# Optimization experiments

Measured on AMD Instinct MI355X. Metric: run time of the kernel, lower is better.

## Reference

```python
import jax, jax.numpy as jnp
import numpy as np

V, TB, L, H, D, HD, FF = 50257, 1024, 6, 12, 768, 64, 4 * 768
B, T = 2, 1024
EOS = 50256


def _layernorm(x, g, b, eps=1e-5):
    mu = x.mean(-1, keepdims=True)
    var = ((x - mu) ** 2).mean(-1, keepdims=True)
    return (x - mu) * jax.lax.rsqrt(var + eps) * g + b


def setup_inputs() -> dict:
    key = jax.random.key(0)
    ks = jax.random.split(key, 10)
    resid_std = 0.02 * (2 * L) ** (-0.5)

    def n(k, shape, std=0.02):
        return (std * jax.random.normal(k, shape)).astype(jnp.float32)

    return {
        "idx": jax.random.randint(ks[0], (B, T), 0, V, dtype=jnp.int32),
        "targets": jax.random.randint(ks[1], (B, T), 0, V, dtype=jnp.int32),
        "token_emb": n(ks[2], (V, D)),           # tied with head
        "pos_emb": n(ks[3], (1, TB, D)),
        "ln1_g": jnp.ones((L, D), jnp.float32),
        "ln1_b": jnp.zeros((L, D), jnp.float32),
        "ln2_g": jnp.ones((L, D), jnp.float32),
        "ln2_b": jnp.zeros((L, D), jnp.float32),
        "W_qkv": n(ks[4], (L, D, 3 * D)),
        "b_qkv": jnp.zeros((L, 3 * D), jnp.float32),
        "W_proj": n(ks[5], (L, D, D), resid_std),
        "b_proj": jnp.zeros((L, D), jnp.float32),
        "W_fc1": n(ks[6], (L, D, FF)),
        "b_fc1": jnp.zeros((L, FF), jnp.float32),
        "W_fc2": n(ks[7], (L, FF, D), resid_std),
        "b_fc2": jnp.zeros((L, D), jnp.float32),
        "lnf_g": jnp.ones((D,), jnp.float32),
        "lnf_b": jnp.zeros((D,), jnp.float32),
    }


def reference(idx, targets, token_emb, pos_emb, ln1_g, ln1_b, ln2_g, ln2_b,
              W_qkv, b_qkv, W_proj, b_proj, W_fc1, b_fc1, W_fc2, b_fc2,
              lnf_g, lnf_b):
    Bc, Tc = idx.shape
    x = token_emb[idx] + pos_emb[:, :Tc, :]  # [B,T,D]; dropout=0 -> identity

    # document-boundary causal mask: same_doc & causal
    is_eos = (idx == EOS).astype(jnp.int32)
    doc_id = jnp.cumsum(is_eos, axis=1) - is_eos          # [B,T]
    same_doc = doc_id[:, :, None] == doc_id[:, None, :]   # [B,T,T]
    causal = jnp.tril(jnp.ones((Tc, Tc), dtype=bool))
    mask = same_doc & causal                               # [B,T,T]
    scale = 1.0 / float(np.sqrt(HD))

    def block(x, p):
        g1, b1, Wq, bq, Wp, bp, g2, b2, Wf1, bf1, Wf2, bf2 = p
        h = _layernorm(x, g1, b1)
        qkv = (h @ Wq + bq).reshape(Bc, Tc, 3, H, HD)
        q = qkv[:, :, 0].transpose(0, 2, 1, 3)  # [B,H,T,hd]
        k = qkv[:, :, 1].transpose(0, 2, 1, 3)
        v = qkv[:, :, 2].transpose(0, 2, 1, 3)
        att = jnp.einsum('bhqd,bhkd->bhqk', q, k) * scale
        att = jnp.where(mask[:, None, :, :], att, -jnp.inf)
        att = jax.nn.softmax(att, axis=-1)
        y = jnp.einsum('bhqk,bhkd->bhqd', att, v)
        y = y.transpose(0, 2, 1, 3).reshape(Bc, Tc, D)
        x = x + (y @ Wp + bp)
        h2 = _layernorm(x, g2, b2)
        x = x + (jax.nn.gelu(h2 @ Wf1 + bf1, approximate=False) @ Wf2 + bf2)
        return x, None

    x, _ = jax.lax.scan(block, x, (ln1_g, ln1_b, W_qkv, b_qkv, W_proj, b_proj,
                                   ln2_g, ln2_b, W_fc1, b_fc1, W_fc2, b_fc2))
    x = _layernorm(x, lnf_g, lnf_b)
    logits = x @ token_emb.T  # tied head, no bias
    logp = jax.nn.log_softmax(logits, axis=-1)
    tgt = targets.astype(jnp.int32)[..., None]
    loss = -jnp.take_along_axis(logp, tgt, axis=-1).mean()
    return logits, loss
```

## Files before the change

### kernel.cpp

```cpp
#include <hip/hip_runtime.h>
#include <hip/hip_bf16.h>
#include <math.h>

#define V_ 50257
#define L_ 6
#define H_ 12
#define D_ 768
#define HD_ 64
#define FF_ 3072
#define B_ 2
#define T_ 1024
#define NTOK (B_*T_)
#define EOS_ 50256
#define QBLK 64
#define KVB 64
#define NS2 393
#define QS3 (3*D_)

typedef __attribute__((ext_vector_type(8))) short s16x8;
typedef __attribute__((ext_vector_type(4))) short s16x4;
typedef __attribute__((ext_vector_type(4))) float f32x4;

__device__ __forceinline__ short f2bf(float f) {
  __hip_bfloat16 h = __float2bfloat16(f);
  return *reinterpret_cast<short*>(&h);
}

__device__ __forceinline__ void gl_lds16(const void* g, void* l) {
  __builtin_amdgcn_global_load_lds(
      (const __attribute__((address_space(1))) unsigned int*)g,
      (__attribute__((address_space(3))) unsigned int*)l, 16, 0, 0);
}

__global__ void k_embed(const int* __restrict__ idx, const float* __restrict__ tok,
                        const float* __restrict__ pos, float* __restrict__ x) {
  int gid = blockIdx.x * blockDim.x + threadIdx.x;
  const int total = NTOK * D_;
  if (gid >= total) return;
  int row = gid / D_;
  int d = gid - row * D_;
  int t = row & (T_ - 1);
  x[gid] = tok[(size_t)idx[row] * D_ + d] + pos[t * D_ + d];
}

__global__ void k_docid(const int* __restrict__ idx, int* __restrict__ doc) {
  int b = threadIdx.x;
  if (b >= B_) return;
  int c = 0;
  for (int t = 0; t < T_; ++t) {
    int e = (idx[b*T_ + t] == EOS_) ? 1 : 0;
    doc[b*T_ + t] = c;
    c += e;
  }
}

__global__ void k_cast_tok(const float* __restrict__ in,
                           __hip_bfloat16* __restrict__ out, long n8) {
  long i = (long)blockIdx.x*blockDim.x + threadIdx.x;
  long stride = (long)gridDim.x*blockDim.x;
  for (; i < n8; i += stride) {
    const float4* src = (const float4*)(in + i*8);
    float4 v0 = src[0], v1 = src[1];
    s16x8 s;
    s[0]=f2bf(v0.x); s[1]=f2bf(v0.y); s[2]=f2bf(v0.z); s[3]=f2bf(v0.w);
    s[4]=f2bf(v1.x); s[5]=f2bf(v1.y); s[6]=f2bf(v1.z); s[7]=f2bf(v1.w);
    *(s16x8*)((short*)out + i*8) = s;
  }
}

__global__ __launch_bounds__(256) void k_ln(
    const float* __restrict__ x, const float* __restrict__ g,
    const float* __restrict__ b, __hip_bfloat16* __restrict__ out) {
  int row = blockIdx.x * 4 + (threadIdx.x >> 6);
  int lane = threadIdx.x & 63;
  const float* xr = x + (size_t)row * D_;
  float4 v[3];
  float s = 0.f;
  #pragma unroll
  for (int i = 0; i < 3; ++i) {
    v[i] = *(const float4*)(xr + lane*4 + i*256);
    s += v[i].x + v[i].y + v[i].z + v[i].w;
  }
  #pragma unroll
  for (int o = 1; o < 64; o <<= 1) s += __shfl_xor(s, o);
  float mu = s * (1.f/D_);
  float var = 0.f;
  #pragma unroll
  for (int i = 0; i < 3; ++i) {
    float a0=v[i].x-mu, a1=v[i].y-mu, a2=v[i].z-mu, a3=v[i].w-mu;
    var += a0*a0 + a1*a1 + a2*a2 + a3*a3;
  }
  #pragma unroll
  for (int o = 1; o < 64; o <<= 1) var += __shfl_xor(var, o);
  float inv = rsqrtf(var * (1.f/D_) + 1e-5f);
  #pragma unroll
  for (int i = 0; i < 3; ++i) {
    int d = lane*4 + i*256;
    float4 gg = *(const float4*)(g + d);
    float4 bb = *(const float4*)(b + d);
    s16x4 o4;
    o4[0] = f2bf((v[i].x-mu)*inv*gg.x + bb.x);
    o4[1] = f2bf((v[i].y-mu)*inv*gg.y + bb.y);
    o4[2] = f2bf((v[i].z-mu)*inv*gg.z + bb.z);
    o4[3] = f2bf((v[i].w-mu)*inv*gg.w + bb.w);
    *(s16x4*)((short*)out + (size_t)row*D_ + d) = o4;
  }
}

__global__ void k_wt(const float* __restrict__ in, __hip_bfloat16* __restrict__ out,
                     int K, int N) {
  __shared__ float tile[32][33];
  int l = blockIdx.z;
  const float* src = in + (size_t)l*K*N;
  __hip_bfloat16* dst = out + (size_t)l*N*K;
  int n0 = blockIdx.x*32, k0 = blockIdx.y*32;
  int tx = threadIdx.x, ty = threadIdx.y;
  #pragma unroll
  for (int i = 0; i < 4; ++i)
    tile[ty + i*8][tx] = src[(size_t)(k0 + ty + i*8)*N + n0 + tx];
  __syncthreads();
  #pragma unroll
  for (int i = 0; i < 4; ++i)
    dst[(size_t)(n0 + ty + i*8)*K + k0 + tx] = __float2bfloat16(tile[tx][ty + i*8]);
}

__global__ __launch_bounds__(256) void k_mfma_nt(
    const __hip_bfloat16* __restrict__ A,
    const __hip_bfloat16* __restrict__ Bh,
    const float* __restrict__ Bf,
    const float* __restrict__ bias,
    const float* resid,
    float* outf, __hip_bfloat16* outh,
    int M, int N, int K, int gelu)
{
  __shared__ __align__(16) short lds_a[2*128*64];
  __shared__ __align__(16) short lds_b[2*64*64];
  const int t = threadIdx.x;
  const int m0 = blockIdx.y * 128;
  const int n0 = blockIdx.x * 64;
  const int lane = t & 63;
  const int wid = t >> 6;
  const int wm = (wid >> 1) * 64;
  const int wn = (wid & 1) * 32;
  const int lrow = lane & 15;
  const int lkb = (lane >> 4) * 16;
  const int wbase = (t & 192) * 16;

  int offA[4][2], offB[2][2];
  #pragma unroll
  for (int f = 0; f < 4; ++f)
    #pragma unroll
    for (int ks = 0; ks < 2; ++ks) {
      int row = wm + f*16 + lrow;
      offA[f][ks] = (row*128 + ks*64 + lkb) ^ ((row & 7) << 4);
    }
  #pragma unroll
  for (int f = 0; f < 2; ++f)
    #pragma unroll
    for (int ks = 0; ks < 2; ++ks) {
      int row = wn + f*16 + lrow;
      offB[f][ks] = (row*128 + ks*64 + lkb) ^ ((row & 7) << 4);
    }

  const char* srcA[4];
  #pragma unroll
  for (int p = 0; p < 4; ++p) {
    int c = p*256 + t;
    int row = c >> 3;
    int colb = (c & 7) << 4;
    srcA[p] = (const char*)A + (size_t)(m0+row)*K*2 + (colb ^ ((row & 7) << 4));
  }
  const char* srcB[2];
  #pragma unroll
  for (int p = 0; p < 2; ++p) {
    int c = p*256 + t;
    int row = c >> 3;
    int colb = (c & 7) << 4;
    srcB[p] = Bh ? ((const char*)Bh + (size_t)(n0+row)*K*2 + (colb ^ ((row & 7) << 4)))
                 : nullptr;
  }

  auto stageA = [&](int boff, int k0) {
    #pragma unroll
    for (int p = 0; p < 4; ++p)
      gl_lds16(srcA[p] + k0*2, (char*)lds_a + boff + p*4096 + wbase);
  };
  auto stageB = [&](int boff, int k0) {
    if (Bh) {
      #pragma unroll
      for (int p = 0; p < 2; ++p)
        gl_lds16(srcB[p] + k0*2, (char*)lds_b + boff + p*4096 + wbase);
    } else {
      #pragma unroll
      for (int p = 0; p < 2; ++p) {
        int c = p*256 + t;
        int row = c >> 3;
        int colb = (c & 7) << 4;
        int gn = n0 + row;
        s16x8 s = {0,0,0,0,0,0,0,0};
        if (gn < N) {
          const char* src = (const char*)Bf + ((size_t)gn*K + k0)*4 + colb*2;
          float4 v0 = *(const float4*)src;
          float4 v1 = *(const float4*)(src + 16);
          s[0]=f2bf(v0.x); s[1]=f2bf(v0.y); s[2]=f2bf(v0.z); s[3]=f2bf(v0.w);
          s[4]=f2bf(v1.x); s[5]=f2bf(v1.y); s[6]=f2bf(v1.z); s[7]=f2bf(v1.w);
        }
        int dst = (row*128 + colb) ^ ((row & 7) << 4);
        *(s16x8*)((char*)lds_b + boff + dst) = s;
      }
    }
  };

  f32x4 acc[4][2];
  #pragma unroll
  for (int i = 0; i < 4; ++i)
    #pragma unroll
    for (int j = 0; j < 2; ++j)
      acc[i][j] = (f32x4){0.f, 0.f, 0.f, 0.f};

  const int nk = K >> 6;
  stageA(0, 0);       stageB(0, 0);
  stageA(1<<14, 64);  stageB(1<<13, 64);
  const bool piped = (Bh != nullptr);
  for (int kt = 0; kt < nk; ++kt) {
    if (piped && kt + 1 < nk) asm volatile("s_waitcnt vmcnt(6)" ::: "memory");
    else                      asm volatile("s_waitcnt vmcnt(0) lgkmcnt(0)" ::: "memory");
    __builtin_amdgcn_s_barrier();
    const int ba = (kt & 1) << 14;
    const int bb = (kt & 1) << 13;
    #pragma unroll
    for (int ks = 0; ks < 2; ++ks) {
      s16x8 af[4], bfr[2];
      #pragma unroll
      for (int f = 0; f < 4; ++f)
        af[f] = *(const s16x8*)((const char*)lds_a + ba + offA[f][ks]);
      #pragma unroll
      for (int f = 0; f < 2; ++f)
        bfr[f] = *(const s16x8*)((const char*)lds_b + bb + offB[f][ks]);
      #pragma unroll
      for (int fm = 0; fm < 4; ++fm)
        #pragma unroll
        for (int fn = 0; fn < 2; ++fn)
          acc[fm][fn] = __builtin_amdgcn_mfma_f32_16x16x32_bf16(
              af[fm], bfr[fn], acc[fm][fn], 0, 0, 0);
    }
    __builtin_amdgcn_s_barrier();
    if (kt + 2 < nk) { stageA(ba, (kt+2)*64); stageB(bb, (kt+2)*64); }
  }
  const int crow = (lane >> 4) * 4;
  #pragma unroll
  for (int fm = 0; fm < 4; ++fm) {
    #pragma unroll
    for (int fn = 0; fn < 2; ++fn) {
      int col = n0 + wn + fn*16 + lrow;
      if (col >= N) continue;
      #pragma unroll
      for (int r = 0; r < 4; ++r) {
        int row = m0 + wm + fm*16 + crow + r;
        float v = acc[fm][fn][r];
        if (bias) v += bias[col];
        if (gelu) v = 0.5f * v * (1.f + erff(v * 0.70710678118654752f));
        if (resid) v += resid[(size_t)row*N + col];
        if (outf) outf[(size_t)row*N + col] = v;
        else      outh[(size_t)row*N + col] = __float2bfloat16(v);
      }
    }
  }
}

__global__ __launch_bounds__(256) void k_mfma_nt64(
    const __hip_bfloat16* __restrict__ A,
    const __hip_bfloat16* __restrict__ Bh,
    const float* __restrict__ bias,
    const float* resid,
    float* outf,
    int M, int N, int K)
{
  __shared__ __align__(16) short lds_a[2][64*64];
  __shared__ __align__(16) short lds_b[2][64*64];
  const int t = threadIdx.x;
  const int m0 = blockIdx.y * 64;
  const int n0 = blockIdx.x * 64;
  const int lane = t & 63;
  const int wid = t >> 6;
  const int wm = (wid >> 1) * 32;
  const int wn = (wid & 1) * 32;
  const int lrow = lane & 15;
  const int lkb = (lane >> 4) * 16;
  const int wbase = (t & 192) * 16;

  auto stage = [&](int buf, int k0) {
    #pragma unroll
    for (int p = 0; p < 2; ++p) {
      int c = p*256 + t;
      int row = c >> 3;
      int colb = (c & 7) << 4;
      const char* srcA = (const char*)A + ((size_t)(m0+row)*K + k0)*2 + (colb ^ ((row & 7) << 4));
      gl_lds16(srcA, (char*)lds_a[buf] + p*4096 + wbase);
    }
    #pragma unroll
    for (int p = 0; p < 2; ++p) {
      int c = p*256 + t;
      int row = c >> 3;
      int colb = (c & 7) << 4;
      const char* srcB = (const char*)Bh + ((size_t)(n0+row)*K + k0)*2 + (colb ^ ((row & 7) << 4));
      gl_lds16(srcB, (char*)lds_b[buf] + p*4096 + wbase);
    }
  };

  f32x4 acc[2][2];
  #pragma unroll
  for (int i = 0; i < 2; ++i)
    #pragma unroll
    for (int j = 0; j < 2; ++j)
      acc[i][j] = (f32x4){0.f, 0.f, 0.f, 0.f};

  const int nk = K >> 6;
  stage(0, 0);
  stage(1, 64);
  for (int kt = 0; kt < nk; ++kt) {
    if (kt + 1 < nk) asm volatile("s_waitcnt vmcnt(4)" ::: "memory");
    else             asm volatile("s_waitcnt vmcnt(0)" ::: "memory");
    __builtin_amdgcn_s_barrier();
    const int cur = kt & 1;
    #pragma unroll
    for (int ks = 0; ks < 2; ++ks) {
      s16x8 af[2], bfr[2];
      #pragma unroll
      for (int f = 0; f < 2; ++f) {
        int row = wm + f*16 + lrow;
        int off = (row*128 + ks*64 + lkb) ^ ((row & 7) << 4);
        af[f] = *(const s16x8*)((const char*)lds_a[cur] + off);
      }
      #pragma unroll
      for (int f = 0; f < 2; ++f) {
        int row = wn + f*16 + lrow;
        int off = (row*128 + ks*64 + lkb) ^ ((row & 7) << 4);
        bfr[f] = *(const s16x8*)((const char*)lds_b[cur] + off);
      }
      #pragma unroll
      for (int fm = 0; fm < 2; ++fm)
        #pragma unroll
        for (int fn = 0; fn < 2; ++fn)
          acc[fm][fn] = __builtin_amdgcn_mfma_f32_16x16x32_bf16(
              af[fm], bfr[fn], acc[fm][fn], 0, 0, 0);
    }
    __builtin_amdgcn_s_barrier();
    if (kt + 2 < nk) stage(cur, (kt+2)*64);
  }
  const int crow = (lane >> 4) * 4;
  #pragma unroll
  for (int fm = 0; fm < 2; ++fm) {
    #pragma unroll
    for (int fn = 0; fn < 2; ++fn) {
      int col = n0 + wn + fn*16 + lrow;
      #pragma unroll
      for (int r = 0; r < 4; ++r) {
        int row = m0 + wm + fm*16 + crow + r;
        float v = acc[fm][fn][r] + bias[col];
        if (resid) v += resid[(size_t)row*N + col];
        outf[(size_t)row*N + col] = v;
      }
    }
  }
}

__global__ __launch_bounds__(512) void k_logits(
    const __hip_bfloat16* __restrict__ A,
    const __hip_bfloat16* __restrict__ Bh,
    const float* __restrict__ Bf,
    float* __restrict__ C,
    float2* __restrict__ part)
{
  __shared__ __align__(16) short lds_a[2*128*64];
  __shared__ __align__(16) short lds_b[2*128*64];
  const int t = threadIdx.x;
  const int bid = blockIdx.x;
  const int lid = (bid & 7) * (NS2*16/8) + (bid >> 3);
  const int m0 = (lid & 15) * 128;
  const int nt = lid >> 4;
  const int n0 = nt * 128;
  const int lane = t & 63;
  const int wid = t >> 6;
  const int wm = (wid >> 2) * 64;
  const int wn = (wid & 3) * 32;
  const int lrow = lane & 15;
  const int lkb = (lane >> 4) * 16;
  const int wbase = (t & 448) * 16;

  int offA[4][2], offB[2][2];
  #pragma unroll
  for (int f = 0; f < 4; ++f)
    #pragma unroll
    for (int ks = 0; ks < 2; ++ks) {
      int row = wm + f*16 + lrow;
      offA[f][ks] = (row*128 + ks*64 + lkb) ^ ((row & 7) << 4);
    }
  #pragma unroll
  for (int f = 0; f < 2; ++f)
    #pragma unroll
    for (int ks = 0; ks < 2; ++ks) {
      int row = wn + f*16 + lrow;
      offB[f][ks] = (row*128 + ks*64 + lkb) ^ ((row & 7) << 4);
    }

  const char* srcA[2];
  const char* srcB[2];
  #pragma unroll
  for (int p = 0; p < 2; ++p) {
    int c = p*512 + t;
    int row = c >> 3;
    int colb = (c & 7) << 4;
    srcA[p] = (const char*)A + (size_t)(m0+row)*768*2 + (colb ^ ((row & 7) << 4));
    srcB[p] = Bh ? ((const char*)Bh + (size_t)(n0+row)*768*2 + (colb ^ ((row & 7) << 4)))
                 : nullptr;
  }

  auto stageA = [&](int boff, int k0) {
    #pragma unroll
    for (int p = 0; p < 2; ++p)
      gl_lds16(srcA[p] + k0*2, (char*)lds_a + boff + p*8192 + wbase);
  };
  auto stageB = [&](int boff, int k0) {
    if (Bh) {
      #pragma unroll
      for (int p = 0; p < 2; ++p)
        gl_lds16(srcB[p] + k0*2, (char*)lds_b + boff + p*8192 + wbase);
    } else {
      #pragma unroll
      for (int p = 0; p < 2; ++p) {
        int c = p*512 + t;
        int row = c >> 3;
        int colb = (c & 7) << 4;
        int gn = n0 + row;
        s16x8 s = {0,0,0,0,0,0,0,0};
        if (gn < V_) {
          const char* src = (const char*)Bf + ((size_t)gn*768 + k0)*4 + colb*2;
          float4 v0 = *(const float4*)src;
          float4 v1 = *(const float4*)(src + 16);
          s[0]=f2bf(v0.x); s[1]=f2bf(v0.y); s[2]=f2bf(v0.z); s[3]=f2bf(v0.w);
          s[4]=f2bf(v1.x); s[5]=f2bf(v1.y); s[6]=f2bf(v1.z); s[7]=f2bf(v1.w);
        }
        int dst = (row*128 + colb) ^ ((row & 7) << 4);
        *(s16x8*)((char*)lds_b + boff + dst) = s;
      }
    }
  };

  f32x4 acc[4][2];
  #pragma unroll
  for (int i = 0; i < 4; ++i)
    #pragma unroll
    for (int j = 0; j < 2; ++j)
      acc[i][j] = (f32x4){0.f, 0.f, 0.f, 0.f};

  stageA(0, 0);       stageB(0, 0);
  stageA(1<<14, 64);  stageB(1<<14, 64);
  const bool piped = (Bh != nullptr);
  for (int kt = 0; kt < 12; ++kt) {
    if (piped && kt + 1 < 12) asm volatile("s_waitcnt vmcnt(4)" ::: "memory");
    else                      asm volatile("s_waitcnt vmcnt(0) lgkmcnt(0)" ::: "memory");
    __builtin_amdgcn_s_barrier();
    const int boff = (kt & 1) << 14;
    #pragma unroll
    for (int ks = 0; ks < 2; ++ks) {
      s16x8 af[4], bfr[2];
      #pragma unroll
      for (int f = 0; f < 4; ++f)
        af[f] = *(const s16x8*)((const char*)lds_a + boff + offA[f][ks]);
      #pragma unroll
      for (int f = 0; f < 2; ++f)
        bfr[f] = *(const s16x8*)((const char*)lds_b + boff + offB[f][ks]);
      #pragma unroll
      for (int fm = 0; fm < 4; ++fm)
        #pragma unroll
        for (int fn = 0; fn < 2; ++fn)
          acc[fm][fn] = __builtin_amdgcn_mfma_f32_16x16x32_bf16(
              af[fm], bfr[fn], acc[fm][fn], 0, 0, 0);
    }
    __builtin_amdgcn_s_barrier();
    if (kt + 2 < 12) { stageA(boff, (kt+2)*64); stageB(boff, (kt+2)*64); }
  }
  const int crow = (lane >> 4) * 4;
  bool valid[2];
  #pragma unroll
  for (int fn = 0; fn < 2; ++fn) valid[fn] = (n0 + wn + fn*16 + lrow) < V_;
  float2* red = (float2*)lds_a;
  #pragma unroll
  for (int fm = 0; fm < 4; ++fm) {
    #pragma unroll
    for (int r = 0; r < 4; ++r) {
      int rit = wm + fm*16 + crow + r;
      int row = m0 + rit;
      float m = -1e30f;
      #pragma unroll
      for (int fn = 0; fn < 2; ++fn) {
        if (valid[fn]) {
          float v = acc[fm][fn][r];
          C[(size_t)row*V_ + n0 + wn + fn*16 + lrow] = v;
          m = fmaxf(m, v);
        }
      }
      #pragma unroll
      for (int o = 1; o < 16; o <<= 1) m = fmaxf(m, __shfl_xor(m, o));
      float s = 0.f;
      #pragma unroll
      for (int fn = 0; fn < 2; ++fn)
        if (valid[fn]) s += __expf(acc[fm][fn][r] - m);
      #pragma unroll
      for (int o = 1; o < 16; o <<= 1) s += __shfl_xor(s, o);
      if (lrow == 0) red[rit*4 + (wid & 3)] = make_float2(m, s);
    }
  }
  __syncthreads();
  if (t < 128) {
    float M = -1e30f, S = 0.f;
    #pragma unroll
    for (int wc = 0; wc < 4; ++wc) {
      float2 p = red[t*4 + wc];
      float mn = fmaxf(M, p.x);
      S = S*__expf(M - mn) + p.y*__expf(p.x - mn);
      M = mn;
    }
    part[(size_t)(m0 + t)*NS2 + nt] = make_float2(M, S);
  }
}

__global__ void k_rowloss2(const float2* __restrict__ part,
                           const float* __restrict__ logits,
                           const int* __restrict__ tgt, float* __restrict__ rl) {
  int row = blockIdx.x;
  int lane = threadIdx.x;
  float M = -1e30f, S = 0.f;
  for (int i = lane; i < NS2; i += 64) {
    float2 p = part[(size_t)row*NS2 + i];
    float mn = fmaxf(M, p.x);
    S = S*__expf(M - mn) + p.y*__expf(p.x - mn);
    M = mn;
  }
  #pragma unroll
  for (int o = 1; o < 64; o <<= 1) {
    float Mo = __shfl_xor(M, o);
    float So = __shfl_xor(S, o);
    float mn = fmaxf(M, Mo);
    S = S*__expf(M - mn) + So*__expf(Mo - mn);
    M = mn;
  }
  if (lane == 0)
    rl[row] = (logf(S) + M) - logits[(size_t)row*V_ + tgt[row]];
}

__global__ __launch_bounds__(256) void k_fattn(
    const __hip_bfloat16* __restrict__ qkv, const int* __restrict__ doc,
    __hip_bfloat16* __restrict__ y)
{
  __shared__ __align__(16) short q_lds[QBLK*64];
  __shared__ __align__(16) short k_lds[2][KVB*64];
  __shared__ __align__(16) short vt_lds[2][64*KVB];
  __shared__ __align__(16) short p_lds[4][16*64];
  __shared__ int doc_lds[T_];
  const int t = threadIdx.x;
  const int lane = t & 63;
  const int w = t >> 6;
  const int q0 = (gridDim.x - 1 - blockIdx.x) * QBLK;
  const int h = blockIdx.y, b = blockIdx.z;
  const int lrow = lane & 15;
  const int lgrp = lane >> 4;
  const int crow = lgrp * 4;
  const int wbase = (t & 192) * 16;
  const short* qp = (const short*)qkv;

  auto stageK = [&](int kv0, int buf) {
    #pragma unroll
    for (int p = 0; p < 2; ++p) {
      int c = p*256 + t;
      int row = c >> 3;
      int colb = (c & 7) << 4;
      const char* src = (const char*)(qp + ((size_t)(b*T_ + kv0 + row))*QS3 + D_ + h*HD_)
                        + (colb ^ ((row & 7) << 4));
      gl_lds16(src, (char*)k_lds[buf] + p*4096 + wbase);
    }
  };

  #pragma unroll
  for (int p = 0; p < 2; ++p) {
    int c = p*256 + t;
    int row = c >> 3;
    int colb = (c & 7) << 4;
    const char* src = (const char*)(qp + ((size_t)(b*T_ + q0 + row))*QS3 + h*HD_)
                      + (colb ^ ((row & 7) << 4));
    gl_lds16(src, (char*)q_lds + p*4096 + wbase);
  }
  #pragma unroll
  for (int i = 0; i < 4; ++i) doc_lds[t + i*256] = doc[b*T_ + t + i*256];
  stageK(0, 0);
  s16x8 vc0, vc1;
  {
    int c0 = t, c1 = 256 + t;
    vc0 = *(const s16x8*)(qp + ((size_t)(b*T_ + (c0>>3)))*QS3 + 2*D_ + h*HD_ + (c0&7)*8);
    vc1 = *(const s16x8*)(qp + ((size_t)(b*T_ + (c1>>3)))*QS3 + 2*D_ + h*HD_ + (c1&7)*8);
  }
  __syncthreads();

  int docq[4];
  #pragma unroll
  for (int r = 0; r < 4; ++r)
    docq[r] = doc_lds[q0 + w*16 + crow + r];

  float m_r[4], l_r[4];
  #pragma unroll
  for (int r = 0; r < 4; ++r) { m_r[r] = -1e30f; l_r[r] = 0.f; }
  f32x4 o[4];
  #pragma unroll
  for (int fd = 0; fd < 4; ++fd) o[fd] = (f32x4){0.f,0.f,0.f,0.f};

  const int ntiles = q0/KVB + 1;
  for (int kt = 0; kt < ntiles; ++kt) {
    const int kv0 = kt * KVB;
    const int cur = kt & 1;
    const bool hn = (kt + 1 < ntiles);
    s16x8 vn0, vn1;
    if (hn) {
      stageK(kv0 + KVB, cur ^ 1);
      int c0 = t, c1 = 256 + t;
      vn0 = *(const s16x8*)(qp + ((size_t)(b*T_ + kv0 + KVB + (c0>>3)))*QS3 + 2*D_ + h*HD_ + (c0&7)*8);
      vn1 = *(const s16x8*)(qp + ((size_t)(b*T_ + kv0 + KVB + (c1>>3)))*QS3 + 2*D_ + h*HD_ + (c1&7)*8);
    }
    {
      int c0 = t, kvr0 = c0 >> 3, d00 = (c0 & 7)*8;
      #pragma unroll
      for (int j = 0; j < 8; ++j) {
        int d = d00 + j;
        int off = (d*128 + kvr0*2) ^ ((d & 7) << 4);
        *(short*)((char*)vt_lds[cur] + off) = vc0[j];
      }
      int c1 = 256 + t, kvr1 = c1 >> 3, d01 = (c1 & 7)*8;
      #pragma unroll
      for (int j = 0; j < 8; ++j) {
        int d = d01 + j;
        int off = (d*128 + kvr1*2) ^ ((d & 7) << 4);
        *(short*)((char*)vt_lds[cur] + off) = vc1[j];
      }
    }
    if (hn) asm volatile("s_waitcnt vmcnt(4)" ::: "memory");
    else    asm volatile("s_waitcnt vmcnt(0)" ::: "memory");
    __builtin_amdgcn_s_barrier();

    f32x4 sfr[4];
    #pragma unroll
    for (int fn = 0; fn < 4; ++fn) sfr[fn] = (f32x4){0.f,0.f,0.f,0.f};
    #pragma unroll
    for (int ks = 0; ks < 2; ++ks) {
      int arow = w*16 + lrow;
      s16x8 af = *(const s16x8*)((const char*)q_lds +
                 ((arow*128 + lgrp*16 + ks*64) ^ ((arow & 7) << 4)));
      #pragma unroll
      for (int fn = 0; fn < 4; ++fn) {
        int brow = fn*16 + lrow;
        s16x8 bf = *(const s16x8*)((const char*)k_lds[cur] +
                   ((brow*128 + lgrp*16 + ks*64) ^ ((brow & 7) << 4)));
        sfr[fn] = __builtin_amdgcn_mfma_f32_16x16x32_bf16(af, bf, sfr[fn], 0, 0, 0);
      }
    }
    int dk[4];
    #pragma unroll
    for (int fn = 0; fn < 4; ++fn) dk[fn] = doc_lds[kv0 + fn*16 + lrow];
    float rowmax[4] = {-1e30f, -1e30f, -1e30f, -1e30f};
    #pragma unroll
    for (int fn = 0; fn < 4; ++fn) {
      int col = kv0 + fn*16 + lrow;
      #pragma unroll
      for (int r = 0; r < 4; ++r) {
        int qrow = q0 + w*16 + crow + r;
        bool ok = (col <= qrow) && (dk[fn] == docq[r]);
        float v = ok ? sfr[fn][r] * 0.125f : -1e30f;
        sfr[fn][r] = v;
        rowmax[r] = fmaxf(rowmax[r], v);
      }
    }
    #pragma unroll
    for (int r = 0; r < 4; ++r) {
      float v = rowmax[r];
      #pragma unroll
      for (int off = 1; off < 16; off <<= 1) v = fmaxf(v, __shfl_xor(v, off));
      rowmax[r] = v;
    }
    float alpha[4], psum[4];
    #pragma unroll
    for (int r = 0; r < 4; ++r) {
      float mn = fmaxf(m_r[r], rowmax[r]);
      alpha[r] = __expf(m_r[r] - mn);
      m_r[r] = mn;
      psum[r] = 0.f;
    }
    #pragma unroll
    for (int fn = 0; fn < 4; ++fn) {
      #pragma unroll
      for (int r = 0; r < 4; ++r) {
        float sv = sfr[fn][r];
        float p = (sv < -5e29f) ? 0.f : __expf(sv - m_r[r]);
        psum[r] += p;
        int rl_ = crow + r;
        int off = (rl_*128 + (fn*16 + lrow)*2) ^ ((rl_ & 7) << 4);
        *(short*)((char*)p_lds[w] + off) = f2bf(p);
      }
    }
    #pragma unroll
    for (int r = 0; r < 4; ++r) {
      float v = psum[r];
      #pragma unroll
      for (int off = 1; off < 16; off <<= 1) v += __shfl_xor(v, off);
      l_r[r] = l_r[r]*alpha[r] + v;
    }
    #pragma unroll
    for (int fd = 0; fd < 4; ++fd)
      #pragma unroll
      for (int r = 0; r < 4; ++r)
        o[fd][r] *= alpha[r];
    #pragma unroll
    for (int ks = 0; ks < 2; ++ks) {
      s16x8 af = *(const s16x8*)((const char*)p_lds[w] +
                 ((lrow*128 + lgrp*16 + ks*64) ^ ((lrow & 7) << 4)));
      #pragma unroll
      for (int fd = 0; fd < 4; ++fd) {
        int brow = fd*16 + lrow;
        s16x8 bf = *(const s16x8*)((const char*)vt_lds[cur] +
                   ((brow*128 + lgrp*16 + ks*64) ^ ((brow & 7) << 4)));
        o[fd] = __builtin_amdgcn_mfma_f32_16x16x32_bf16(af, bf, o[fd], 0, 0, 0);
      }
    }
    __builtin_amdgcn_s_barrier();
    vc0 = vn0; vc1 = vn1;
  }
  #pragma unroll
  for (int r = 0; r < 4; ++r) {
    float inv = 1.f / l_r[r];
    int rowg = b*T_ + q0 + w*16 + crow + r;
    #pragma unroll
    for (int fd = 0; fd < 4; ++fd) {
      int col = h*HD_ + fd*16 + lrow;
      y[(size_t)rowg*D_ + col] = __float2bfloat16(o[fd][r] * inv);
    }
  }
}

__global__ void k_rowloss(const float* __restrict__ logits,
                          const int* __restrict__ tgt, float* __restrict__ rl) {
  __shared__ float red[4];
  int row = blockIdx.x;
  const float* lr = logits + (size_t)row * V_;
  int tid = threadIdx.x;
  float m = -1e30f;
  for (int v = tid; v < V_; v += 256) m = fmaxf(m, lr[v]);
  #pragma unroll
  for (int o = 1; o < 64; o <<= 1) m = fmaxf(m, __shfl_xor(m, o));
  if ((tid & 63) == 0) red[tid >> 6] = m;
  __syncthreads();
  m = fmaxf(fmaxf(red[0], red[1]), fmaxf(red[2], red[3]));
  __syncthreads();
  float s = 0.f;
  for (int v = tid; v < V_; v += 256) s += __expf(lr[v] - m);
  #pragma unroll
  for (int o = 1; o < 64; o <<= 1) s += __shfl_xor(s, o);
  if ((tid & 63) == 0) red[tid >> 6] = s;
  __syncthreads();
  if (tid == 0) {
    s = red[0]+red[1]+red[2]+red[3];
    rl[row] = (logf(s) + m) - lr[tgt[row]];
  }
}

__global__ void k_loss(const float* __restrict__ rl, float* __restrict__ out) {
  __shared__ float red[4];
  int tid = threadIdx.x;
  float s = 0.f;
  for (int i = tid; i < NTOK; i += 256) s += rl[i];
  #pragma unroll
  for (int o = 1; o < 64; o <<= 1) s += __shfl_xor(s, o);
  if ((tid & 63) == 0) red[tid >> 6] = s;
  __syncthreads();
  if (tid == 0) {
    s = red[0]+red[1]+red[2]+red[3];
    out[0] = s / (float)NTOK;
  }
}

extern "C" void kernel_launch(void* const* d_in, const int* in_sizes, int n_in,
                              void* d_out, int out_size, void* d_ws, size_t ws_size,
                              hipStream_t stream) {
  const int*   idx   = (const int*)d_in[0];
  const int*   tgt   = (const int*)d_in[1];
  const float* tok   = (const float*)d_in[2];
  const float* pos   = (const float*)d_in[3];
  const float* ln1_g = (const float*)d_in[4];
  const float* ln1_b = (const float*)d_in[5];
  const float* ln2_g = (const float*)d_in[6];
  const float* ln2_b = (const float*)d_in[7];
  const float* W_qkv = (const float*)d_in[8];
  const float* b_qkv = (const float*)d_in[9];
  const float* W_proj= (const float*)d_in[10];
  const float* b_proj= (const float*)d_in[11];
  const float* W_fc1 = (const float*)d_in[12];
  const float* b_fc1 = (const float*)d_in[13];
  const float* W_fc2 = (const float*)d_in[14];
  const float* b_fc2 = (const float*)d_in[15];
  const float* lnf_g = (const float*)d_in[16];
  const float* lnf_b = (const float*)d_in[17];

  float* out = (float*)d_out;

  char* ob = (char*)d_out;
  float*           x    = (float*)(ob + 0);
  __hip_bfloat16*  qkv  = (__hip_bfloat16*)(ob + (size_t)6291456);
  __hip_bfloat16*  y    = (__hip_bfloat16*)(ob + (size_t)15728640);
  __hip_bfloat16*  tff  = (__hip_bfloat16*)(ob + (size_t)18874368);
  __hip_bfloat16*  WTq  = (__hip_bfloat16*)(ob + (size_t)40894464);
  __hip_bfloat16*  WTp  = (__hip_bfloat16*)(ob + (size_t)62128128);
  __hip_bfloat16*  WT1  = (__hip_bfloat16*)(ob + (size_t)69206016);
  __hip_bfloat16*  WT2  = (__hip_bfloat16*)(ob + (size_t)97517568);

  char* wb = (char*)d_ws;
  __hip_bfloat16* h    = (__hip_bfloat16*)(wb + 0);
  int*    doc  = (int*)  (wb + (size_t)3145728);
  float*  rl   = (float*)(wb + (size_t)3153920);
  float2* part = (float2*)(wb + (size_t)3162112);
  __hip_bfloat16* tokh = (__hip_bfloat16*)(wb + (size_t)9601024);
  const size_t ws_need_part = (size_t)9601024;
  const size_t ws_need_tokh = (size_t)9601024 + 77194752 + 131072;
  const bool fused_loss = (ws_size >= ws_need_part);
  const bool use_tokh   = (ws_size >= ws_need_tokh);

  dim3 tb(32, 8);
  k_wt<<<dim3(2304/32, 768/32, L_), tb, 0, stream>>>(W_qkv,  WTq,  768, 2304);
  k_wt<<<dim3( 768/32, 768/32, L_), tb, 0, stream>>>(W_proj, WTp,  768,  768);
  k_wt<<<dim3(3072/32, 768/32, L_), tb, 0, stream>>>(W_fc1,  WT1,  768, 3072);
  k_wt<<<dim3( 768/32,3072/32, L_), tb, 0, stream>>>(W_fc2,  WT2, 3072,  768);
  if (use_tokh)
    k_cast_tok<<<2048, 256, 0, stream>>>(tok, tokh, (long)V_*768/8);

  k_embed<<<(NTOK*D_ + 255)/256, 256, 0, stream>>>(idx, tok, pos, x);
  k_docid<<<1, 64, 0, stream>>>(idx, doc);

  for (int l = 0; l < L_; ++l) {
    k_ln<<<NTOK/4, 256, 0, stream>>>(x, ln1_g + l*D_, ln1_b + l*D_, h);
    k_mfma_nt<<<dim3(2304/64, NTOK/128), 256, 0, stream>>>(
        h, WTq + (size_t)l*2304*768, nullptr, b_qkv + (size_t)l*2304, nullptr,
        nullptr, qkv, NTOK, 2304, 768, 0);
    k_fattn<<<dim3(T_/QBLK, H_, B_), 256, 0, stream>>>(qkv, doc, y);
    k_mfma_nt64<<<dim3(768/64, NTOK/64), 256, 0, stream>>>(
        y, WTp + (size_t)l*768*768, b_proj + (size_t)l*768, x, x,
        NTOK, 768, 768);
    k_ln<<<NTOK/4, 256, 0, stream>>>(x, ln2_g + l*D_, ln2_b + l*D_, h);
    k_mfma_nt<<<dim3(3072/64, NTOK/128), 256, 0, stream>>>(
        h, WT1 + (size_t)l*3072*768, nullptr, b_fc1 + (size_t)l*3072, nullptr,
        nullptr, tff, NTOK, 3072, 768, 1);
    k_mfma_nt64<<<dim3(768/64, NTOK/64), 256, 0, stream>>>(
        tff, WT2 + (size_t)l*768*3072, b_fc2 + (size_t)l*768, x, x,
        NTOK, 768, 3072);
  }
  k_ln<<<NTOK/4, 256, 0, stream>>>(x, lnf_g, lnf_b, h);

  if (fused_loss) {
    k_logits<<<NS2*16, 512, 0, stream>>>(
        h, use_tokh ? tokh : nullptr, tok, out, part);
    k_rowloss2<<<NTOK, 64, 0, stream>>>(part, out, tgt, rl);
  } else {
    k_mfma_nt<<<dim3((V_ + 63)/64, NTOK/128), 256, 0, stream>>>(
        h, nullptr, tok, nullptr, nullptr, out, nullptr, NTOK, V_, 768, 0);
    k_rowloss<<<NTOK, 256, 0, stream>>>(out, tgt, rl);
  }
  k_loss<<<1, 256, 0, stream>>>(rl, out + (size_t)NTOK*V_);
}
```

Before: 1.487 ms.

## Retile logits GEMM to 64x128 with 256 threads and triple-buffered LDS

Shrinks the logits kernel's block tile from 128x128 (512 threads) to 64x128 (256 threads) and doubles the grid. LDS staging goes from double to triple buffering, so the second barrier per k-step disappears and the next tile's loads are issued before the MFMAs. The fp32-cast fallback path inside the kernel is removed, so the fused path now runs only when the bf16 token table fits in the workspace. The smaller tile means more blocks and more reloads of the B operand, in exchange for possibly better occupancy and overlap.

```diff
diff --git a/kernel.cpp b/kernel.cpp
--- a/kernel.cpp
+++ b/kernel.cpp
@@ -365,39 +365,38 @@
   }
 }
 
-__global__ __launch_bounds__(512) void k_logits(
+__global__ __launch_bounds__(256) void k_logits(
     const __hip_bfloat16* __restrict__ A,
     const __hip_bfloat16* __restrict__ Bh,
-    const float* __restrict__ Bf,
     float* __restrict__ C,
     float2* __restrict__ part)
 {
-  __shared__ __align__(16) short lds_a[2*128*64];
-  __shared__ __align__(16) short lds_b[2*128*64];
+  __shared__ __align__(16) short lds_a[3*64*64];
+  __shared__ __align__(16) short lds_b[3*128*64];
   const int t = threadIdx.x;
   const int bid = blockIdx.x;
-  const int lid = (bid & 7) * (NS2*16/8) + (bid >> 3);
-  const int m0 = (lid & 15) * 128;
-  const int nt = lid >> 4;
+  const int lid = (bid & 7) * (NS2*32/8) + (bid >> 3);
+  const int m0 = (lid & 31) * 64;
+  const int nt = lid >> 5;
   const int n0 = nt * 128;
   const int lane = t & 63;
   const int wid = t >> 6;
-  const int wm = (wid >> 2) * 64;
-  const int wn = (wid & 3) * 32;
+  const int wm = (wid >> 1) * 32;
+  const int wn = (wid & 1) * 64;
   const int lrow = lane & 15;
   const int lkb = (lane >> 4) * 16;
-  const int wbase = (t & 448) * 16;
-
-  int offA[4][2], offB[2][2];
-  #pragma unroll
-  for (int f = 0; f < 4; ++f)
+  const int wbase = (t & 192) * 16;
+
+  int offA[2][2], offB[4][2];
+  #pragma unroll
+  for (int f = 0; f < 2; ++f)
     #pragma unroll
     for (int ks = 0; ks < 2; ++ks) {
       int row = wm + f*16 + lrow;
       offA[f][ks] = (row*128 + ks*64 + lkb) ^ ((row & 7) << 4);
     }
   #pragma unroll
-  for (int f = 0; f < 2; ++f)
+  for (int f = 0; f < 4; ++f)
     #pragma unroll
     for (int ks = 0; ks < 2; ++ks) {
       int row = wn + f*16 + lrow;
@@ -405,96 +404,86 @@
     }
 
   const char* srcA[2];
-  const char* srcB[2];
   #pragma unroll
   for (int p = 0; p < 2; ++p) {
-    int c = p*512 + t;
+    int c = p*256 + t;
     int row = c >> 3;
     int colb = (c & 7) << 4;
     srcA[p] = (const char*)A + (size_t)(m0+row)*768*2 + (colb ^ ((row & 7) << 4));
-    srcB[p] = Bh ? ((const char*)Bh + (size_t)(n0+row)*768*2 + (colb ^ ((row & 7) << 4)))
-                 : nullptr;
-  }
-
-  auto stageA = [&](int boff, int k0) {
+  }
+  const char* srcB[4];
+  #pragma unroll
+  for (int p = 0; p < 4; ++p) {
+    int c = p*256 + t;
+    int row = c >> 3;
+    int colb = (c & 7) << 4;
+    srcB[p] = (const char*)Bh + (size_t)(n0+row)*768*2 + (colb ^ ((row & 7) << 4));
+  }
+
+  auto stage = [&](int buf, int k0) {
+    const int ab = buf * 8192;
+    const int bb = buf * 16384;
     #pragma unroll
     for (int p = 0; p < 2; ++p)
-      gl_lds16(srcA[p] + k0*2, (char*)lds_a + boff + p*8192 + wbase);
+      gl_lds16(srcA[p] + k0*2, (char*)lds_a + ab + p*4096 + wbase);
+    #pragma unroll
+    for (int p = 0; p < 4; ++p)
+      gl_lds16(srcB[p] + k0*2, (char*)lds_b + bb + p*4096 + wbase);
   };
-  auto stageB = [&](int boff, int k0) {
-    if (Bh) {
-      #pragma unroll
-      for (int p = 0; p < 2; ++p)
-        gl_lds16(srcB[p] + k0*2, (char*)lds_b + boff + p*8192 + wbase);
-    } else {
-      #pragma unroll
-      for (int p = 0; p < 2; ++p) {
-        int c = p*512 + t;
-        int row = c >> 3;
-        int colb = (c & 7) << 4;
-        int gn = n0 + row;
-        s16x8 s = {0,0,0,0,0,0,0,0};
-        if (gn < V_) {
-          const char* src = (const char*)Bf + ((size_t)gn*768 + k0)*4 + colb*2;
-          float4 v0 = *(const float4*)src;
-          float4 v1 = *(const float4*)(src + 16);
-          s[0]=f2bf(v0.x); s[1]=f2bf(v0.y); s[2]=f2bf(v0.z); s[3]=f2bf(v0.w);
-          s[4]=f2bf(v1.x); s[5]=f2bf(v1.y); s[6]=f2bf(v1.z); s[7]=f2bf(v1.w);
-        }
-        int dst = (row*128 + colb) ^ ((row & 7) << 4);
-        *(s16x8*)((char*)lds_b + boff + dst) = s;
-      }
-    }
-  };
-
-  f32x4 acc[4][2];
-  #pragma unroll
-  for (int i = 0; i < 4; ++i)
-    #pragma unroll
-    for (int j = 0; j < 2; ++j)
+
+  f32x4 acc[2][4];
+  #pragma unroll
+  for (int i = 0; i < 2; ++i)
+    #pragma unroll
+    for (int j = 0; j < 4; ++j)
       acc[i][j] = (f32x4){0.f, 0.f, 0.f, 0.f};
 
-  stageA(0, 0);       stageB(0, 0);
-  stageA(1<<14, 64);  stageB(1<<14, 64);
-  const bool piped = (Bh != nullptr);
+  stage(0, 0);
+  stage(1, 64);
+  #pragma unroll
   for (int kt = 0; kt < 12; ++kt) {
-    if (piped && kt + 1 < 12) asm volatile("s_waitcnt vmcnt(4)" ::: "memory");
-    else                      asm volatile("s_waitcnt vmcnt(0) lgkmcnt(0)" ::: "memory");
+    if (kt + 1 < 12) asm volatile("s_waitcnt vmcnt(6)" ::: "memory");
+    else             asm volatile("s_waitcnt vmcnt(0)" ::: "memory");
     __builtin_amdgcn_s_barrier();
-    const int boff = (kt & 1) << 14;
+    const int cb = kt % 3;
+    const int ab = cb * 8192;
+    const int bb = cb * 16384;
+    s16x8 af[2][2], bfr[4][2];
     #pragma unroll
     for (int ks = 0; ks < 2; ++ks) {
-      s16x8 af[4], bfr[2];
+      #pragma unroll
+      for (int f = 0; f < 2; ++f)
+        af[f][ks] = *(const s16x8*)((const char*)lds_a + ab + offA[f][ks]);
       #pragma unroll
       for (int f = 0; f < 4; ++f)
-        af[f] = *(const s16x8*)((const char*)lds_a + boff + offA[f][ks]);
-      #pragma unroll
-      for (int f = 0; f < 2; ++f)
-        bfr[f] = *(const s16x8*)((const char*)lds_b + boff + offB[f][ks]);
-      #pragma unroll
-      for (int fm = 0; fm < 4; ++fm)
+        bfr[f][ks] = *(const s16x8*)((const char*)lds_b + bb + offB[f][ks]);
+    }
+    if (kt + 2 < 12) stage((kt + 2) % 3, (kt + 2) * 64);
+    #pragma unroll
+    for (int ks = 0; ks < 2; ++ks)
+      #pragma unroll
+      for (int fm = 0; fm < 2; ++fm)
         #pragma unroll
-        for (int fn = 0; fn < 2; ++fn)
+        for (int fn = 0; fn < 4; ++fn)
           acc[fm][fn] = __builtin_amdgcn_mfma_f32_16x16x32_bf16(
-              af[fm], bfr[fn], acc[fm][fn], 0, 0, 0);
-    }
-    __builtin_amdgcn_s_barrier();
-    if (kt + 2 < 12) { stageA(boff, (kt+2)*64); stageB(boff, (kt+2)*64); }
-  }
+              af[fm][ks], bfr[fn][ks], acc[fm][fn], 0, 0, 0);
+  }
+  __syncthreads();
+
   const int crow = (lane >> 4) * 4;
-  bool valid[2];
-  #pragma unroll
-  for (int fn = 0; fn < 2; ++fn) valid[fn] = (n0 + wn + fn*16 + lrow) < V_;
+  bool valid[4];
+  #pragma unroll
+  for (int fn = 0; fn < 4; ++fn) valid[fn] = (n0 + wn + fn*16 + lrow) < V_;
   float2* red = (float2*)lds_a;
   #pragma unroll
-  for (int fm = 0; fm < 4; ++fm) {
+  for (int fm = 0; fm < 2; ++fm) {
     #pragma unroll
     for (int r = 0; r < 4; ++r) {
       int rit = wm + fm*16 + crow + r;
       int row = m0 + rit;
       float m = -1e30f;
       #pragma unroll
-      for (int fn = 0; fn < 2; ++fn) {
+      for (int fn = 0; fn < 4; ++fn) {
         if (valid[fn]) {
           float v = acc[fm][fn][r];
           C[(size_t)row*V_ + n0 + wn + fn*16 + lrow] = v;
@@ -505,24 +494,19 @@
       for (int o = 1; o < 16; o <<= 1) m = fmaxf(m, __shfl_xor(m, o));
       float s = 0.f;
       #pragma unroll
-      for (int fn = 0; fn < 2; ++fn)
+      for (int fn = 0; fn < 4; ++fn)
         if (valid[fn]) s += __expf(acc[fm][fn][r] - m);
       #pragma unroll
       for (int o = 1; o < 16; o <<= 1) s += __shfl_xor(s, o);
-      if (lrow == 0) red[rit*4 + (wid & 3)] = make_float2(m, s);
+      if (lrow == 0) red[rit*2 + (wid & 1)] = make_float2(m, s);
     }
   }
   __syncthreads();
-  if (t < 128) {
-    float M = -1e30f, S = 0.f;
-    #pragma unroll
-    for (int wc = 0; wc < 4; ++wc) {
-      float2 p = red[t*4 + wc];
-      float mn = fmaxf(M, p.x);
-      S = S*__expf(M - mn) + p.y*__expf(p.x - mn);
-      M = mn;
-    }
-    part[(size_t)(m0 + t)*NS2 + nt] = make_float2(M, S);
+  if (t < 64) {
+    float2 a = red[t*2], b = red[t*2 + 1];
+    float mn = fmaxf(a.x, b.x);
+    float S = a.y*__expf(a.x - mn) + b.y*__expf(b.x - mn);
+    part[(size_t)(m0 + t)*NS2 + nt] = make_float2(mn, S);
   }
 }
 
@@ -825,10 +809,8 @@
   float*  rl   = (float*)(wb + (size_t)3153920);
   float2* part = (float2*)(wb + (size_t)3162112);
   __hip_bfloat16* tokh = (__hip_bfloat16*)(wb + (size_t)9601024);
-  const size_t ws_need_part = (size_t)9601024;
   const size_t ws_need_tokh = (size_t)9601024 + 77194752 + 131072;
-  const bool fused_loss = (ws_size >= ws_need_part);
-  const bool use_tokh   = (ws_size >= ws_need_tokh);
+  const bool use_tokh = (ws_size >= ws_need_tokh);
 
   dim3 tb(32, 8);
   k_wt<<<dim3(2304/32, 768/32, L_), tb, 0, stream>>>(W_qkv,  WTq,  768, 2304);
@@ -860,9 +842,8 @@
   }
   k_ln<<<NTOK/4, 256, 0, stream>>>(x, lnf_g, lnf_b, h);
 
-  if (fused_loss) {
-    k_logits<<<NS2*16, 512, 0, stream>>>(
-        h, use_tokh ? tokh : nullptr, tok, out, part);
+  if (use_tokh) {
+    k_logits<<<NS2*32, 256, 0, stream>>>(h, tokh, out, part);
     k_rowloss2<<<NTOK, 64, 0, stream>>>(part, out, tgt, rl);
   } else {
     k_mfma_nt<<<dim3((V_ + 63)/64, NTOK/128), 256, 0, stream>>>(
```

Measured after the change: 1.586 ms. 1.07x slower.
